# Kernel tuning notes

Hardware: AMD Instinct MI355X
Metric: run time of the kernel (lower is better)

## Reference

```python
import jax, jax.numpy as jnp
import numpy as np

N = 100000      # nodes
E = 3200000     # edges (avg degree 32)
IN = 256        # in_channels
HID = 32        # hidden (hard-coded in module)
OUT = 40        # out_channels / classes
BN_EPS = 1e-5


def gcn_conv(x, W, b, src, dst, n):
    # PyG GCNConv: h = x @ W; add self-loops; symmetric norm D^-1/2 A D^-1/2; aggregate; + bias
    h = x @ W                                   # [n, d_out]
    loop = jnp.arange(n)
    s = jnp.concatenate([src, loop])            # [E+n]
    d = jnp.concatenate([dst, loop])
    deg = jax.ops.segment_sum(jnp.ones_like(d, dtype=h.dtype), d, num_segments=n)
    dinv = jnp.where(deg > 0, jax.lax.rsqrt(deg), 0.0)
    norm = dinv[s] * dinv[d]                    # [E+n]
    msg = h[s] * norm[:, None]                  # gather + scale
    return jax.ops.segment_sum(msg, d, num_segments=n) + b


def setup_inputs() -> dict:
    key = jax.random.key(0)
    k = jax.random.split(key, 4)
    x = jax.random.normal(k[0], (N, IN), dtype=jnp.float32)
    edge_index = jax.random.randint(k[1], (2, E), 0, N, dtype=jnp.int64)
    W1 = jax.random.normal(k[2], (IN, HID), dtype=jnp.float32) / np.float32(np.sqrt(IN))
    b1 = jnp.zeros((HID,), jnp.float32)
    W2 = jax.random.normal(k[3], (HID, OUT), dtype=jnp.float32) / np.float32(np.sqrt(HID))
    b2 = jnp.zeros((OUT,), jnp.float32)
    return {"x": x, "edge_index": edge_index, "W1": W1, "b1": b1, "W2": W2, "b2": b2}


def reference(x, edge_index, W1, b1, W2, b2):
    src, dst = edge_index[0], edge_index[1]
    h = jax.nn.elu(gcn_conv(x, W1, b1, src, dst, N))
    # BatchNorm1d created fresh each forward: batch stats, gamma=1, beta=0 (biased var)
    mean = jnp.mean(h, axis=0)
    var = jnp.mean((h - mean) ** 2, axis=0)
    h = (h - mean) * jax.lax.rsqrt(var + BN_EPS)
    h = jax.nn.relu(h)
    # Dropout(p=0.2): identity in eval / deterministic reference
    out = gcn_conv(h, W2, b2, src, dst, N)
    return jax.nn.log_softmax(out, axis=-1)
```

## Files before the change

### kernel.cpp

```cpp
#include <hip/hip_runtime.h>
#include <math.h>

typedef unsigned int uint;
typedef unsigned short ushort;
typedef float v2f __attribute__((ext_vector_type(2)));

__device__ __forceinline__ v2f fp8lo_to_f32(uint u) {
    return __builtin_amdgcn_cvt_pk_f32_fp8((int)u, false);
}
__device__ __forceinline__ v2f fp8hi_to_f32(uint u) {
    return __builtin_amdgcn_cvt_pk_f32_fp8((int)u, true);
}
__device__ __forceinline__ ushort f32x2_to_fp8(float a, float b) {
    return (ushort)(__builtin_amdgcn_cvt_pk_fp8_f32(a, b, 0, false) & 0xffff);
}

#define UNPACK8(r, f)                                                  \
    {                                                                  \
        v2f p0_ = fp8lo_to_f32((r).x), p1_ = fp8hi_to_f32((r).x);      \
        v2f p2_ = fp8lo_to_f32((r).y), p3_ = fp8hi_to_f32((r).y);      \
        f[0] += p0_.x; f[1] += p0_.y; f[2] += p1_.x; f[3] += p1_.y;    \
        f[4] += p2_.x; f[5] += p2_.y; f[6] += p3_.x; f[7] += p3_.y;    \
    }

#define NBU 49
#define CELL 9216
#define SCAP2 9216
#define BUCK_CAP (8 * SCAP2)

__global__ __launch_bounds__(256) void k_bin(
    const int* __restrict__ src, const int* __restrict__ dst,
    int* __restrict__ cur, uint* __restrict__ ebuf, int E) {
    __shared__ int hist[NBU], base_[NBU], off[NBU];
    int tid = threadIdx.x;
    if (tid < NBU) { hist[tid] = 0; off[tid] = 0; }
    __syncthreads();
    int e0 = blockIdx.x * 4096 + tid;
    int s_[16], d_[16];
#pragma unroll
    for (int j = 0; j < 16; ++j) {
        int e = e0 + j * 256;
        if (e < E) {
            s_[j] = src[e]; d_[j] = dst[e];
            atomicAdd(&hist[d_[j] >> 11], 1);
        } else d_[j] = -1;
    }
    __syncthreads();
    int seg = blockIdx.x & 7;
    if (tid < NBU && hist[tid])
        base_[tid] = atomicAdd(&cur[tid * 8 + seg], hist[tid]);
    __syncthreads();
#pragma unroll
    for (int j = 0; j < 16; ++j) {
        if (d_[j] >= 0) {
            int b = d_[j] >> 11;
            int p = base_[b] + atomicAdd(&off[b], 1);
            if (p < CELL)
                ebuf[(size_t)(b * 8 + seg) * CELL + p] =
                    ((uint)(d_[j] & 2047) << 17) | (uint)s_[j];
        }
    }
}

__global__ __launch_bounds__(256) void k_sort2(
    const int* __restrict__ cur, const uint* __restrict__ ebuf,
    uint* __restrict__ csr, int* __restrict__ rowstart, int* __restrict__ deg,
    float* __restrict__ dinv, int n) {
    __shared__ int hist[256];
    __shared__ int wsum[4];
    int tid = threadIdx.x;
    int b = blockIdx.x >> 3;
    uint sl = blockIdx.x & 7;
    hist[tid] = 0;
    __syncthreads();
    int lens[8];
    for (int s = 0; s < 8; ++s) {
        int len = cur[b * 8 + s]; if (len > CELL) len = CELL; lens[s] = len;
        const uint* ep = ebuf + (size_t)(b * 8 + s) * CELL;
        int i = tid;
        for (; i + 768 < len; i += 1024) {
            uint v0 = ep[i], v1 = ep[i + 256], v2 = ep[i + 512], v3 = ep[i + 768];
            if ((v0 >> 25) == sl) atomicAdd(&hist[(v0 >> 17) & 255], 1);
            if ((v1 >> 25) == sl) atomicAdd(&hist[(v1 >> 17) & 255], 1);
            if ((v2 >> 25) == sl) atomicAdd(&hist[(v2 >> 17) & 255], 1);
            if ((v3 >> 25) == sl) atomicAdd(&hist[(v3 >> 17) & 255], 1);
        }
        for (; i < len; i += 256) {
            uint v = ep[i];
            if ((v >> 25) == sl) atomicAdd(&hist[(v >> 17) & 255], 1);
        }
    }
    __syncthreads();
    int c = hist[tid];
    int lane = tid & 63, w = tid >> 6;
    int incl = c;
#pragma unroll
    for (int o = 1; o < 64; o <<= 1) {
        int t = __shfl_up(incl, o, 64);
        if (lane >= o) incl += t;
    }
    if (lane == 63) wsum[w] = incl;
    __syncthreads();
    int add = 0;
#pragma unroll
    for (int k = 0; k < 4; ++k) if (k < w) add += wsum[k];
    int excl = incl - c + add;
    int sliceBase = (int)blockIdx.x * SCAP2;
    int node = b * 2048 + (int)sl * 256 + tid;
    if (node < n) {
        deg[node] = c;
        dinv[node] = rsqrtf((float)c + 1.0f);
        rowstart[node] = sliceBase + excl;
    }
    __syncthreads();
    hist[tid] = excl;
    __syncthreads();
    for (int s = 0; s < 8; ++s) {
        const uint* ep = ebuf + (size_t)(b * 8 + s) * CELL;
        int len = lens[s];
        int i = tid;
        for (; i + 768 < len; i += 1024) {
            uint v0 = ep[i], v1 = ep[i + 256], v2 = ep[i + 512], v3 = ep[i + 768];
            if ((v0 >> 25) == sl) {
                int p = atomicAdd(&hist[(v0 >> 17) & 255], 1);
                if (p < SCAP2) csr[sliceBase + p] = v0 & 0x1FFFFu;
            }
            if ((v1 >> 25) == sl) {
                int p = atomicAdd(&hist[(v1 >> 17) & 255], 1);
                if (p < SCAP2) csr[sliceBase + p] = v1 & 0x1FFFFu;
            }
            if ((v2 >> 25) == sl) {
                int p = atomicAdd(&hist[(v2 >> 17) & 255], 1);
                if (p < SCAP2) csr[sliceBase + p] = v2 & 0x1FFFFu;
            }
            if ((v3 >> 25) == sl) {
                int p = atomicAdd(&hist[(v3 >> 17) & 255], 1);
                if (p < SCAP2) csr[sliceBase + p] = v3 & 0x1FFFFu;
            }
        }
        for (; i < len; i += 256) {
            uint v = ep[i];
            if ((v >> 25) == sl) {
                int p = atomicAdd(&hist[(v >> 17) & 255], 1);
                if (p < SCAP2) csr[sliceBase + p] = v & 0x1FFFFu;
            }
        }
    }
}


__global__ __launch_bounds__(256) void k_gemm1(
    const float* __restrict__ x, const float* __restrict__ W,
    const float* __restrict__ dinv, ushort* __restrict__ h8, int n) {
    __shared__ float part[4 * 32 * 64];
    int lane = threadIdx.x & 63;
    int wv = __builtin_amdgcn_readfirstlane(threadIdx.x >> 6);
    int node0 = blockIdx.x * 64;
    int node = node0 + lane;
    int koff = wv * 64;

    float acc[32];
#pragma unroll
    for (int c = 0; c < 32; ++c) acc[c] = 0.f;
    if (node < n) {
        const float4* xr = (const float4*)(x + (size_t)node * 256 + koff);
#pragma unroll 4
        for (int j4 = 0; j4 < 16; ++j4) {
            float4 xv = xr[j4];
            const float* w0 = W + (koff + j4 * 4) * 32;
#pragma unroll
            for (int c = 0; c < 32; ++c) acc[c] += xv.x * w0[c];
#pragma unroll
            for (int c = 0; c < 32; ++c) acc[c] += xv.y * w0[32 + c];
#pragma unroll
            for (int c = 0; c < 32; ++c) acc[c] += xv.z * w0[64 + c];
#pragma unroll
            for (int c = 0; c < 32; ++c) acc[c] += xv.w * w0[96 + c];
        }
    }
    float* pw = part + wv * 2048 + lane;
#pragma unroll
    for (int c = 0; c < 32; ++c) pw[c * 64] = acc[c];
    __syncthreads();

    int rn = threadIdx.x >> 2;
    int cq = threadIdx.x & 3;
    int dnode = node0 + rn;
    if (dnode < n) {
        float di = dinv[dnode];
        ushort us[4];
#pragma unroll
        for (int half = 0; half < 4; ++half) {
            float v0 = 0.f, v1 = 0.f;
#pragma unroll
            for (int w = 0; w < 4; ++w) {
                v0 += part[w * 2048 + (cq * 8 + half * 2 + 0) * 64 + rn];
                v1 += part[w * 2048 + (cq * 8 + half * 2 + 1) * 64 + rn];
            }
            us[half] = f32x2_to_fp8(v0 * di, v1 * di);
        }
        uint2 p;
        p.x = (uint)us[0] | ((uint)us[1] << 16);
        p.y = (uint)us[2] | ((uint)us[3] << 16);
        *(uint2*)(h8 + (size_t)dnode * 16 + cq * 4) = p;
    }
}

__global__ __launch_bounds__(256) void k_agg1(
    const ushort* __restrict__ hs, const int* __restrict__ deg,
    const int* __restrict__ rowstart, const uint* __restrict__ csr,
    const float* __restrict__ dinv, const float* __restrict__ b1,
    ushort* __restrict__ y, float* __restrict__ partials, int n) {
    int tid = threadIdx.x;
    int l4 = tid & 3;
    int g  = tid >> 2;
    int d  = blockIdx.x * 64 + g;
    float sa[8], qa[8];
#pragma unroll
    for (int j = 0; j < 8; ++j) { sa[j] = 0.f; qa[j] = 0.f; }
    if (d < n) {
        float a[8], c[8];
#pragma unroll
        for (int j = 0; j < 8; ++j) { a[j] = 0.f; c[j] = 0.f; }
        uint2 sr = *((const uint2*)(hs + (size_t)d * 16) + l4);
        UNPACK8(sr, a);
        const uint* row = csr + rowstart[d];
        int end = deg[d];
        int k = 0;
        for (; k + 4 <= end; k += 4) {
            uint s0 = row[k], s1 = row[k+1], s2 = row[k+2], s3 = row[k+3];
            uint2 r0 = *((const uint2*)(hs + (size_t)s0 * 16) + l4);
            uint2 r1 = *((const uint2*)(hs + (size_t)s1 * 16) + l4);
            uint2 r2 = *((const uint2*)(hs + (size_t)s2 * 16) + l4);
            uint2 r3 = *((const uint2*)(hs + (size_t)s3 * 16) + l4);
            UNPACK8(r0, a); UNPACK8(r1, c);
            UNPACK8(r2, a); UNPACK8(r3, c);
        }
        for (; k < end; ++k) {
            uint2 r = *((const uint2*)(hs + (size_t)row[k] * 16) + l4);
            UNPACK8(r, a);
        }
        float di = dinv[d];
        float4 bA = *(const float4*)(b1 + l4 * 8);
        float4 bB = *(const float4*)(b1 + l4 * 8 + 4);
        float bv[8] = {bA.x, bA.y, bA.z, bA.w, bB.x, bB.y, bB.z, bB.w};
        float vv[8];
#pragma unroll
        for (int j = 0; j < 8; ++j) {
            float v = di * (a[j] + c[j]) + bv[j];
            v = v > 0.f ? v : expm1f(v);
            vv[j] = v; sa[j] = v; qa[j] = v * v;
        }
        ushort u0 = f32x2_to_fp8(vv[0], vv[1]);
        ushort u1 = f32x2_to_fp8(vv[2], vv[3]);
        ushort u2 = f32x2_to_fp8(vv[4], vv[5]);
        ushort u3 = f32x2_to_fp8(vv[6], vv[7]);
        uint2 pw;
        pw.x = (uint)u0 | ((uint)u1 << 16);
        pw.y = (uint)u2 | ((uint)u3 << 16);
        *((uint2*)(y + (size_t)d * 16) + l4) = pw;
    }
#pragma unroll
    for (int m = 4; m <= 32; m <<= 1) {
#pragma unroll
        for (int j = 0; j < 8; ++j) {
            sa[j] += __shfl_xor(sa[j], m, 64);
            qa[j] += __shfl_xor(qa[j], m, 64);
        }
    }
    __shared__ float wred[4][4][16];
    int lane = tid & 63, wv = tid >> 6;
    if (lane < 4) {
#pragma unroll
        for (int j = 0; j < 8; ++j) {
            wred[wv][lane][j]     = sa[j];
            wred[wv][lane][8 + j] = qa[j];
        }
    }
    __syncthreads();
    if (tid < 64) {
        int l4g = tid >> 4, slot = tid & 15;
        partials[(size_t)blockIdx.x * 64 + tid] =
            wred[0][l4g][slot] + wred[1][l4g][slot] +
            wred[2][l4g][slot] + wred[3][l4g][slot];
    }
}

__global__ __launch_bounds__(1024) void k_red(
    const float* __restrict__ partials, float* __restrict__ stats, int nblk) {
    __shared__ float red[1024];
    int t = threadIdx.x;
    int j = t & 63, w = t >> 6;
    float a = 0.f;
    for (int i = w; i < nblk; i += 16) a += partials[(size_t)i * 64 + j];
    red[t] = a;
    __syncthreads();
    if (t < 64) {
        float v = 0.f;
#pragma unroll
        for (int kk = 0; kk < 16; ++kk) v += red[kk * 64 + t];
        int l4g = t >> 4, slot = t & 15, c = l4g * 8 + (slot & 7);
        stats[(slot < 8) ? c : (32 + c)] = v;
    }
}

__global__ void k_bn2(const ushort* __restrict__ y, const float* __restrict__ stats,
                      const float* __restrict__ dinv, ushort* __restrict__ h2s, int n) {
    int t = blockIdx.x * blockDim.x + threadIdx.x;
    if (t >= n * 16) return;
    int i = t >> 4, c2 = (t & 15) * 2;
    float invn = 1.0f / (float)n;
    float m0 = stats[c2] * invn,    m1 = stats[c2+1] * invn;
    float v0 = stats[32+c2] * invn - m0*m0;
    float v1 = stats[33+c2] * invn - m1*m1;
    float s0 = rsqrtf(v0 + 1e-5f), s1 = rsqrtf(v1 + 1e-5f);
    float di = dinv[i];
    v2f u = fp8lo_to_f32(y[t]);
    float a = (u.x - m0) * s0; a = a > 0.f ? a : 0.f; a *= di;
    float b = (u.y - m1) * s1; b = b > 0.f ? b : 0.f; b *= di;
    h2s[t] = f32x2_to_fp8(a, b);
}

__global__ __launch_bounds__(256) void k_agg2(
    const ushort* __restrict__ h2s, const int* __restrict__ deg,
    const int* __restrict__ rowstart, const uint* __restrict__ csr,
    const float* __restrict__ dinv, const float* __restrict__ W2,
    const float* __restrict__ b2, float* __restrict__ out, int n) {
    __shared__ float w2s[1280];
    __shared__ float b2s[40];
    __shared__ float tb[64][33];
    int tid = threadIdx.x;
    for (int t = tid; t < 1280; t += 256) w2s[t] = W2[t];
    if (tid < 40) b2s[tid] = b2[tid];
    int l4 = tid & 3, g = tid >> 2;
    int d = blockIdx.x * 64 + g;
    if (d < n) {
        float a[8], c[8];
#pragma unroll
        for (int j = 0; j < 8; ++j) { a[j] = 0.f; c[j] = 0.f; }
        uint2 sr = *((const uint2*)(h2s + (size_t)d * 16) + l4);
        UNPACK8(sr, a);
        const uint* row = csr + rowstart[d];
        int end = deg[d];
        int k = 0;
        for (; k + 4 <= end; k += 4) {
            uint s0 = row[k], s1 = row[k+1], s2 = row[k+2], s3 = row[k+3];
            uint2 r0 = *((const uint2*)(h2s + (size_t)s0 * 16) + l4);
            uint2 r1 = *((const uint2*)(h2s + (size_t)s1 * 16) + l4);
            uint2 r2 = *((const uint2*)(h2s + (size_t)s2 * 16) + l4);
            uint2 r3 = *((const uint2*)(h2s + (size_t)s3 * 16) + l4);
            UNPACK8(r0, a); UNPACK8(r1, c);
            UNPACK8(r2, a); UNPACK8(r3, c);
        }
        for (; k < end; ++k) {
            uint2 r = *((const uint2*)(h2s + (size_t)row[k] * 16) + l4);
            UNPACK8(r, a);
        }
        float di = dinv[d];
#pragma unroll
        for (int j = 0; j < 8; ++j) tb[g][l4 * 8 + j] = di * (a[j] + c[j]);
    }
    __syncthreads();
    float o[10];
    const float* bp = b2s + l4 * 10;
#pragma unroll
    for (int m = 0; m < 10; ++m) o[m] = bp[m];
#pragma unroll
    for (int cc = 0; cc < 32; ++cc) {
        float tc = tb[g][cc];
        const float* wr = w2s + cc * 40 + l4 * 10;
#pragma unroll
        for (int m = 0; m < 10; ++m) o[m] += tc * wr[m];
    }
    float mx = o[0];
#pragma unroll
    for (int m = 1; m < 10; ++m) mx = fmaxf(mx, o[m]);
    mx = fmaxf(mx, __shfl_xor(mx, 1, 64));
    mx = fmaxf(mx, __shfl_xor(mx, 2, 64));
    float s = 0.f;
#pragma unroll
    for (int m = 0; m < 10; ++m) s += __expf(o[m] - mx);
    s += __shfl_xor(s, 1, 64);
    s += __shfl_xor(s, 2, 64);
    float lse = mx + __logf(s);
    if (d < n) {
        float* r = out + (size_t)d * 40 + l4 * 10;
#pragma unroll
        for (int m = 0; m < 10; m += 2) {
            float2 wv;
            wv.x = o[m] - lse; wv.y = o[m+1] - lse;
            *(float2*)(r + m) = wv;
        }
    }
}


extern "C" void kernel_launch(void* const* d_in, const int* in_sizes, int n_in,
                              void* d_out, int out_size, void* d_ws, size_t ws_size,
                              hipStream_t stream) {
    const float* x  = (const float*)d_in[0];
    const int*   ei = (const int*)d_in[1];
    const float* W1 = (const float*)d_in[2];
    const float* b1 = (const float*)d_in[3];
    const float* W2 = (const float*)d_in[4];
    const float* b2 = (const float*)d_in[5];

    int n = in_sizes[0] / 256;
    int E = in_sizes[1] / 2;
    const int* src = ei;
    const int* dst = ei + E;

    char*   base    = (char*)d_ws;
    ushort* hs8     = (ushort*)base;
    ushort* y       = (ushort*)(base + (size_t)n * 32);
    ushort* h2s     = (ushort*)(base + (size_t)n * 64);
    float*  dinv    = (float*) (base + (size_t)n * 96);
    int*    deg     = (int*)   (base + (size_t)n * 100);
    int*    rowstart= (int*)   (base + (size_t)n * 104);
    float*  stats   = (float*) (base + (size_t)n * 108);
    int*    cur     = (int*)   (base + (size_t)n * 108 + 256);
    float*  partials= (float*) (base + (size_t)n * 108 + 2304);
    uint*   ebuf    = (uint*)  (base + (size_t)n * 108 + 2304 + 524288);
    size_t  ebufB   = (size_t)NBU * 8 * CELL * 4;
    uint*   csr     = (uint*)  ((char*)ebuf + ebufB);
    float*  out     = (float*)d_out;

    const int B = 256;
    int nb64 = (n + 63) / 64;

    hipMemsetAsync(cur, 0, NBU * 8 * sizeof(int), stream);

    k_bin  <<<(E + 4095) / 4096, B, 0, stream>>>(src, dst, cur, ebuf, E);
    k_sort2<<<NBU * 8, B, 0, stream>>>(cur, ebuf, csr, rowstart, deg, dinv, n);

    k_gemm1<<<(n + 63) / 64, B, 0, stream>>>(x, W1, dinv, hs8, n);
    k_agg1 <<<nb64, B, 0, stream>>>(hs8, deg, rowstart, csr, dinv, b1, y,
                                    partials, n);
    k_red  <<<1, 1024, 0, stream>>>(partials, stats, nb64);

    k_bn2<<<(n * 16 + B - 1) / B, B, 0, stream>>>(y, stats, dinv, h2s, n);

    k_agg2<<<nb64, B, 0, stream>>>(h2s, deg, rowstart, csr, dinv, W2, b2, out, n);
}
```

Before: 427.7 us.

## Add second binning pass so CSR sort blocks read only their own edges

Replaces the single sort pass, where each of 8 slice blocks rescanned all edges of a 2048-node bucket and discarded most of them, with a two-level radix: k_bin2 splits each bucket segment into 16 sub-buckets of 128 nodes. k_sort3 then builds CSR per 128-node group from only its own edges. This removes the eightfold redundant reading of the edge buffer. In exchange it adds one kernel launch, an extra write and read of all edges through the subcell buffer, and fixed per-slot capacities that drop edges if a 128-node slot overflows.

```diff
diff --git a/kernel.cpp b/kernel.cpp
--- a/kernel.cpp
+++ b/kernel.cpp
@@ -24,9 +24,10 @@
     }
 
 #define NBU 49
-#define CELL 9216
-#define SCAP2 9216
-#define BUCK_CAP (8 * SCAP2)
+#define NSEG 4
+#define CELL 17408
+#define SUBCAP 1280
+#define CSRCAP 4608
 
 __global__ __launch_bounds__(256) void k_bin(
     const int* __restrict__ src, const int* __restrict__ dst,
@@ -46,9 +47,9 @@
         } else d_[j] = -1;
     }
     __syncthreads();
-    int seg = blockIdx.x & 7;
+    int seg = blockIdx.x & 3;
     if (tid < NBU && hist[tid])
-        base_[tid] = atomicAdd(&cur[tid * 8 + seg], hist[tid]);
+        base_[tid] = atomicAdd(&cur[tid * NSEG + seg], hist[tid]);
     __syncthreads();
 #pragma unroll
     for (int j = 0; j < 16; ++j) {
@@ -56,42 +57,81 @@
             int b = d_[j] >> 11;
             int p = base_[b] + atomicAdd(&off[b], 1);
             if (p < CELL)
-                ebuf[(size_t)(b * 8 + seg) * CELL + p] =
+                ebuf[(size_t)(b * NSEG + seg) * CELL + p] =
                     ((uint)(d_[j] & 2047) << 17) | (uint)s_[j];
         }
     }
 }
 
-__global__ __launch_bounds__(256) void k_sort2(
+__global__ __launch_bounds__(256) void k_bin2(
     const int* __restrict__ cur, const uint* __restrict__ ebuf,
+    uint* __restrict__ subcell, int* __restrict__ slotlen) {
+    __shared__ int curs[16], sbase[16];
+    int tid = threadIdx.x;
+    int b = blockIdx.x >> 2, seg = blockIdx.x & 3;
+    if (tid < 16) {
+        int sb = ((b * 16 + tid) * NSEG + seg) * SUBCAP;
+        sbase[tid] = sb;
+        curs[tid] = sb;
+    }
+    __syncthreads();
+    int len = cur[b * NSEG + seg]; if (len > CELL) len = CELL;
+    const uint* ep = ebuf + (size_t)(b * NSEG + seg) * CELL;
+    int i = tid;
+    for (; i + 768 < len; i += 1024) {
+        uint v0 = ep[i], v1 = ep[i + 256], v2 = ep[i + 512], v3 = ep[i + 768];
+        int u0 = (v0 >> 24) & 15, u1 = (v1 >> 24) & 15;
+        int u2 = (v2 >> 24) & 15, u3 = (v3 >> 24) & 15;
+        int p0 = atomicAdd(&curs[u0], 1);
+        if (p0 - sbase[u0] < SUBCAP) subcell[p0] = v0;
+        int p1 = atomicAdd(&curs[u1], 1);
+        if (p1 - sbase[u1] < SUBCAP) subcell[p1] = v1;
+        int p2 = atomicAdd(&curs[u2], 1);
+        if (p2 - sbase[u2] < SUBCAP) subcell[p2] = v2;
+        int p3 = atomicAdd(&curs[u3], 1);
+        if (p3 - sbase[u3] < SUBCAP) subcell[p3] = v3;
+    }
+    for (; i < len; i += 256) {
+        uint v = ep[i];
+        int u = (v >> 24) & 15;
+        int p = atomicAdd(&curs[u], 1);
+        if (p - sbase[u] < SUBCAP) subcell[p] = v;
+    }
+    __syncthreads();
+    if (tid < 16) {
+        int c = curs[tid] - sbase[tid];
+        slotlen[(b * 16 + tid) * NSEG + seg] = c < SUBCAP ? c : SUBCAP;
+    }
+}
+
+__global__ __launch_bounds__(256) void k_sort3(
+    const int* __restrict__ slotlen, const uint* __restrict__ subcell,
     uint* __restrict__ csr, int* __restrict__ rowstart, int* __restrict__ deg,
     float* __restrict__ dinv, int n) {
-    __shared__ int hist[256];
-    __shared__ int wsum[4];
+    __shared__ int hist[128];
+    __shared__ int wtot;
     int tid = threadIdx.x;
-    int b = blockIdx.x >> 3;
-    uint sl = blockIdx.x & 7;
-    hist[tid] = 0;
-    __syncthreads();
-    int lens[8];
-    for (int s = 0; s < 8; ++s) {
-        int len = cur[b * 8 + s]; if (len > CELL) len = CELL; lens[s] = len;
-        const uint* ep = ebuf + (size_t)(b * 8 + s) * CELL;
+    int bs = blockIdx.x;
+    if (tid < 128) hist[tid] = 0;
+    __syncthreads();
+    int lens[NSEG];
+    const uint* sp = subcell + (size_t)bs * NSEG * SUBCAP;
+    for (int s = 0; s < NSEG; ++s) {
+        int len = slotlen[bs * NSEG + s];
+        lens[s] = len;
+        const uint* ep = sp + s * SUBCAP;
         int i = tid;
         for (; i + 768 < len; i += 1024) {
             uint v0 = ep[i], v1 = ep[i + 256], v2 = ep[i + 512], v3 = ep[i + 768];
-            if ((v0 >> 25) == sl) atomicAdd(&hist[(v0 >> 17) & 255], 1);
-            if ((v1 >> 25) == sl) atomicAdd(&hist[(v1 >> 17) & 255], 1);
-            if ((v2 >> 25) == sl) atomicAdd(&hist[(v2 >> 17) & 255], 1);
-            if ((v3 >> 25) == sl) atomicAdd(&hist[(v3 >> 17) & 255], 1);
-        }
-        for (; i < len; i += 256) {
-            uint v = ep[i];
-            if ((v >> 25) == sl) atomicAdd(&hist[(v >> 17) & 255], 1);
-        }
-    }
-    __syncthreads();
-    int c = hist[tid];
+            atomicAdd(&hist[(v0 >> 17) & 127], 1);
+            atomicAdd(&hist[(v1 >> 17) & 127], 1);
+            atomicAdd(&hist[(v2 >> 17) & 127], 1);
+            atomicAdd(&hist[(v3 >> 17) & 127], 1);
+        }
+        for (; i < len; i += 256) atomicAdd(&hist[(ep[i] >> 17) & 127], 1);
+    }
+    __syncthreads();
+    int c = (tid < 128) ? hist[tid] : 0;
     int lane = tid & 63, w = tid >> 6;
     int incl = c;
 #pragma unroll
@@ -99,51 +139,38 @@
         int t = __shfl_up(incl, o, 64);
         if (lane >= o) incl += t;
     }
-    if (lane == 63) wsum[w] = incl;
-    __syncthreads();
-    int add = 0;
-#pragma unroll
-    for (int k = 0; k < 4; ++k) if (k < w) add += wsum[k];
-    int excl = incl - c + add;
-    int sliceBase = (int)blockIdx.x * SCAP2;
-    int node = b * 2048 + (int)sl * 256 + tid;
-    if (node < n) {
+    if (w == 0 && lane == 63) wtot = incl;
+    __syncthreads();
+    int excl = incl - c + ((w == 1) ? wtot : 0);
+    int csrBase = bs * CSRCAP;
+    int node = bs * 128 + tid;
+    if (tid < 128 && node < n) {
         deg[node] = c;
         dinv[node] = rsqrtf((float)c + 1.0f);
-        rowstart[node] = sliceBase + excl;
-    }
-    __syncthreads();
-    hist[tid] = excl;
-    __syncthreads();
-    for (int s = 0; s < 8; ++s) {
-        const uint* ep = ebuf + (size_t)(b * 8 + s) * CELL;
+        rowstart[node] = csrBase + excl;
+    }
+    __syncthreads();
+    if (tid < 128) hist[tid] = excl;
+    __syncthreads();
+    for (int s = 0; s < NSEG; ++s) {
+        const uint* ep = sp + s * SUBCAP;
         int len = lens[s];
         int i = tid;
         for (; i + 768 < len; i += 1024) {
             uint v0 = ep[i], v1 = ep[i + 256], v2 = ep[i + 512], v3 = ep[i + 768];
-            if ((v0 >> 25) == sl) {
-                int p = atomicAdd(&hist[(v0 >> 17) & 255], 1);
-                if (p < SCAP2) csr[sliceBase + p] = v0 & 0x1FFFFu;
-            }
-            if ((v1 >> 25) == sl) {
-                int p = atomicAdd(&hist[(v1 >> 17) & 255], 1);
-                if (p < SCAP2) csr[sliceBase + p] = v1 & 0x1FFFFu;
-            }
-            if ((v2 >> 25) == sl) {
-                int p = atomicAdd(&hist[(v2 >> 17) & 255], 1);
-                if (p < SCAP2) csr[sliceBase + p] = v2 & 0x1FFFFu;
-            }
-            if ((v3 >> 25) == sl) {
-                int p = atomicAdd(&hist[(v3 >> 17) & 255], 1);
-                if (p < SCAP2) csr[sliceBase + p] = v3 & 0x1FFFFu;
-            }
+            int p0 = atomicAdd(&hist[(v0 >> 17) & 127], 1);
+            csr[csrBase + p0] = v0 & 0x1FFFFu;
+            int p1 = atomicAdd(&hist[(v1 >> 17) & 127], 1);
+            csr[csrBase + p1] = v1 & 0x1FFFFu;
+            int p2 = atomicAdd(&hist[(v2 >> 17) & 127], 1);
+            csr[csrBase + p2] = v2 & 0x1FFFFu;
+            int p3 = atomicAdd(&hist[(v3 >> 17) & 127], 1);
+            csr[csrBase + p3] = v3 & 0x1FFFFu;
         }
         for (; i < len; i += 256) {
             uint v = ep[i];
-            if ((v >> 25) == sl) {
-                int p = atomicAdd(&hist[(v >> 17) & 255], 1);
-                if (p < SCAP2) csr[sliceBase + p] = v & 0x1FFFFu;
-            }
+            int p = atomicAdd(&hist[(v >> 17) & 127], 1);
+            csr[csrBase + p] = v & 0x1FFFFu;
         }
     }
 }
@@ -419,19 +446,24 @@
     int*    rowstart= (int*)   (base + (size_t)n * 104);
     float*  stats   = (float*) (base + (size_t)n * 108);
     int*    cur     = (int*)   (base + (size_t)n * 108 + 256);
-    float*  partials= (float*) (base + (size_t)n * 108 + 2304);
-    uint*   ebuf    = (uint*)  (base + (size_t)n * 108 + 2304 + 524288);
-    size_t  ebufB   = (size_t)NBU * 8 * CELL * 4;
-    uint*   csr     = (uint*)  ((char*)ebuf + ebufB);
+    int*    slotlen = (int*)   (base + (size_t)n * 108 + 1280);
+    float*  partials= (float*) (base + (size_t)n * 108 + 13824);
+    uint*   ebuf    = (uint*)  (base + (size_t)n * 108 + 538112);
+    size_t  ebufB   = (size_t)NBU * NSEG * CELL * 4;
+    uint*   subcell = (uint*)  ((char*)ebuf + ebufB);
+    size_t  subB    = (size_t)NBU * 16 * NSEG * SUBCAP * 4;
+    uint*   csr     = (uint*)  ((char*)subcell + subB);
     float*  out     = (float*)d_out;
 
     const int B = 256;
     int nb64 = (n + 63) / 64;
 
-    hipMemsetAsync(cur, 0, NBU * 8 * sizeof(int), stream);
+    hipMemsetAsync(cur, 0, NBU * NSEG * sizeof(int), stream);
 
     k_bin  <<<(E + 4095) / 4096, B, 0, stream>>>(src, dst, cur, ebuf, E);
-    k_sort2<<<NBU * 8, B, 0, stream>>>(cur, ebuf, csr, rowstart, deg, dinv, n);
+    k_bin2 <<<NBU * NSEG, B, 0, stream>>>(cur, ebuf, subcell, slotlen);
+    k_sort3<<<NBU * 16, B, 0, stream>>>(slotlen, subcell, csr, rowstart, deg,
+                                        dinv, n);
 
     k_gemm1<<<(n + 63) / 64, B, 0, stream>>>(x, W1, dinv, hs8, n);
     k_agg1 <<<nb64, B, 0, stream>>>(hs8, deg, rowstart, csr, dinv, b1, y,
```

After: 374.4 us. 1.14x faster.
